# Optimization experiments

Measured on AMD Instinct MI355X. Metric: run time of the kernel, lower is better.

Reference implementation:

```python
import jax, jax.numpy as jnp
import numpy as np

TOP_K = 2


def setup_inputs() -> dict:
    key = jax.random.key(0)
    k0, k1, k2, k3, k4 = jax.random.split(key, 5)
    B, S, H, I, E = 4, 2048, 1024, 2816, 8
    s_h = 1.0 / np.sqrt(H)
    s_i = 1.0 / np.sqrt(I)
    return {
        "x": jax.random.normal(k0, (B, S, H), jnp.float32),
        # nn.Linear weights are stored as [out_features, in_features]
        "w_router": jax.random.normal(k1, (E, H), jnp.float32) * s_h,   # gate: H -> E
        "w_gate": jax.random.normal(k2, (E, I, H), jnp.float32) * s_h,  # per-expert gate_proj
        "w_up": jax.random.normal(k3, (E, I, H), jnp.float32) * s_h,    # per-expert up_proj
        "w_down": jax.random.normal(k4, (E, H, I), jnp.float32) * s_i,  # per-expert down_proj
    }


def reference(x, w_router, w_gate, w_up, w_down):
    B, S, H = x.shape
    E = w_router.shape[0]
    xf = x.reshape(-1, H)                      # [T, H], T = B*S

    # --- Router: softmax over experts, top-k, renormalize weights ---
    logits = jnp.einsum("th,eh->te", xf, w_router)        # [T, E]
    probs = jax.nn.softmax(logits, axis=-1)
    topw, topi = jax.lax.top_k(probs, TOP_K)              # [T, k]
    topw = topw / jnp.sum(topw, axis=-1, keepdims=True)

    # Per-token combine weight for each expert: sum_k w[t,k] * 1[idx[t,k]==e]
    onehot = (topi[..., None] == jnp.arange(E)).astype(x.dtype)  # [T, k, E]
    combine = jnp.einsum("tk,tke->te", topw, onehot)             # [T, E]

    # --- Experts: SwiGLU MLP per expert on all tokens, masked combine ---
    # (masked-dense in the original == gather-compute mathematically,
    # since silu(0)*0 = 0 and the projections have no bias)
    gate = jax.nn.silu(jnp.einsum("th,eih->eti", xf, w_gate))    # [E, T, I]
    up = jnp.einsum("th,eih->eti", xf, w_up)                     # [E, T, I]
    down = jnp.einsum("eti,ehi->eth", gate * up, w_down)         # [E, T, H]

    out = jnp.einsum("eth,te->th", down, combine)                # [T, H]
    return out.reshape(B, S, H)
```

## Files before the change

### kernel.cpp

```cpp
#include <hip/hip_runtime.h>

#define TT 8192
#define HD 1024
#define ID 2816
#define NE 8
#define NID2 (2*ID)

typedef __attribute__((ext_vector_type(8))) short short8;
typedef __attribute__((ext_vector_type(4))) float f32x4;

#define WS_TOP2I 0
#define WS_TOP2W 65536
#define WS_CNT   131072
#define WS_OFF   131136
#define WS_CUR   131200
#define WS_TMAP  131328
#define WS_SLOTW 196864
#define WS_T2S   262400
#define WS_XB    1048576ULL
#define WS_WGU   (WS_XB  + 16777216ULL)
#define WS_WDB   (WS_WGU + 92274688ULL)
#define WS_ACT   (WS_WDB + 46137344ULL)

__device__ __forceinline__ unsigned int pack_bf2(float lo, float hi) {
  unsigned int ul = __builtin_bit_cast(unsigned int, lo) + 0x8000u;
  unsigned int uh = __builtin_bit_cast(unsigned int, hi) + 0x8000u;
  return (uh & 0xffff0000u) | (ul >> 16);
}

__device__ __forceinline__ unsigned short f2bf(float f) {
  unsigned int u = __builtin_bit_cast(unsigned int, f);
  return (unsigned short)((u + 0x8000u) >> 16);
}

__device__ __forceinline__ float bf2f(unsigned short b) {
  unsigned int u = ((unsigned int)b) << 16;
  return __builtin_bit_cast(float, u);
}

__device__ __forceinline__ void gload16(const void* g, void* l) {
  __builtin_amdgcn_global_load_lds(
      (const __attribute__((address_space(1))) unsigned int*)g,
      (__attribute__((address_space(3))) unsigned int*)l, 16, 0, 0);
}

__global__ __launch_bounds__(256) void router_kernel(
    const float* __restrict__ x, const float* __restrict__ wr,
    int* __restrict__ top2i, float* __restrict__ top2w,
    unsigned short* __restrict__ xb)
{
  int tid  = threadIdx.x;
  int lane = tid & 63;
  int t    = blockIdx.x * 4 + (tid >> 6);

  const float4* xp = (const float4*)(x + (size_t)t * HD + lane * 16);
  float4 xv[4];
  #pragma unroll
  for (int j = 0; j < 4; ++j) xv[j] = xp[j];

  uint4 v0, v1;
  v0.x = pack_bf2(xv[0].x, xv[0].y); v0.y = pack_bf2(xv[0].z, xv[0].w);
  v0.z = pack_bf2(xv[1].x, xv[1].y); v0.w = pack_bf2(xv[1].z, xv[1].w);
  v1.x = pack_bf2(xv[2].x, xv[2].y); v1.y = pack_bf2(xv[2].z, xv[2].w);
  v1.z = pack_bf2(xv[3].x, xv[3].y); v1.w = pack_bf2(xv[3].z, xv[3].w);
  uint4* xrow = (uint4*)(xb + (size_t)t * HD + lane * 16);
  xrow[0] = v0; xrow[1] = v1;

  float acc[NE];
  #pragma unroll
  for (int e = 0; e < NE; ++e) {
    const float4* wp = (const float4*)(wr + (size_t)e * HD + lane * 16);
    float s = 0.f;
    #pragma unroll
    for (int j = 0; j < 4; ++j) {
      float4 w = wp[j];
      s += xv[j].x * w.x + xv[j].y * w.y + xv[j].z * w.z + xv[j].w * w.w;
    }
    acc[e] = s;
  }
  #pragma unroll
  for (int d = 1; d < 64; d <<= 1) {
    #pragma unroll
    for (int e = 0; e < NE; ++e) acc[e] += __shfl_xor(acc[e], d, 64);
  }
  int   i0 = 0; float m0 = acc[0];
  #pragma unroll
  for (int e = 1; e < NE; ++e) if (acc[e] > m0) { m0 = acc[e]; i0 = e; }
  int   i1 = -1; float m1 = -3.4e38f;
  #pragma unroll
  for (int e = 0; e < NE; ++e) if (e != i0 && acc[e] > m1) { m1 = acc[e]; i1 = e; }

  float e1 = __expf(m1 - m0);
  float w0 = 1.f / (1.f + e1);
  float w1 = e1 * w0;

  if (lane == 0) {
    top2i[2 * t] = i0;  top2i[2 * t + 1] = i1;
    top2w[2 * t] = w0;  top2w[2 * t + 1] = w1;
  }
}

__global__ __launch_bounds__(256) void count_scan_kernel(
    const int* __restrict__ top2i,
    int* __restrict__ counts, int* __restrict__ offsets, int* __restrict__ cursors)
{
  __shared__ int s_cnt[NE];
  int tid = threadIdx.x;
  if (tid < NE) s_cnt[tid] = 0;
  __syncthreads();

  int c0=0,c1=0,c2=0,c3=0,c4=0,c5=0,c6=0,c7=0;
  for (int t = tid; t < TT; t += 256) {
    int e0 = top2i[2 * t], e1 = top2i[2 * t + 1];
    c0 += __popcll(__ballot(e0 == 0)) + __popcll(__ballot(e1 == 0));
    c1 += __popcll(__ballot(e0 == 1)) + __popcll(__ballot(e1 == 1));
    c2 += __popcll(__ballot(e0 == 2)) + __popcll(__ballot(e1 == 2));
    c3 += __popcll(__ballot(e0 == 3)) + __popcll(__ballot(e1 == 3));
    c4 += __popcll(__ballot(e0 == 4)) + __popcll(__ballot(e1 == 4));
    c5 += __popcll(__ballot(e0 == 5)) + __popcll(__ballot(e1 == 5));
    c6 += __popcll(__ballot(e0 == 6)) + __popcll(__ballot(e1 == 6));
    c7 += __popcll(__ballot(e0 == 7)) + __popcll(__ballot(e1 == 7));
  }
  if ((tid & 63) == 0) {
    atomicAdd(&s_cnt[0], c0); atomicAdd(&s_cnt[1], c1);
    atomicAdd(&s_cnt[2], c2); atomicAdd(&s_cnt[3], c3);
    atomicAdd(&s_cnt[4], c4); atomicAdd(&s_cnt[5], c5);
    atomicAdd(&s_cnt[6], c6); atomicAdd(&s_cnt[7], c7);
  }
  __syncthreads();
  if (tid == 0) {
    int run = 0;
    #pragma unroll
    for (int e = 0; e < NE; ++e) {
      counts[e] = s_cnt[e]; offsets[e] = run; cursors[e] = run; run += s_cnt[e];
    }
    offsets[NE] = run;
  }
}

__global__ __launch_bounds__(256) void place_kernel(
    const int* __restrict__ top2i, const float* __restrict__ top2w,
    int* __restrict__ cursors,
    int* __restrict__ token_map, float* __restrict__ slot_w, int* __restrict__ tok2slot)
{
  int tid  = threadIdx.x;
  int lane = tid & 63;
  int t    = blockIdx.x * 256 + tid;

  #pragma unroll
  for (int k = 0; k < 2; ++k) {
    int   e = top2i[2 * t + k];
    float w = top2w[2 * t + k];
    #pragma unroll
    for (int ee = 0; ee < NE; ++ee) {
      unsigned long long m = __ballot(e == ee);
      if (e == ee) {
        int leader = __ffsll((long long)m) - 1;
        int pre    = __popcll(m & ((1ull << lane) - 1ull));
        int base   = 0;
        if (lane == leader) base = atomicAdd(&cursors[ee], (int)__popcll(m));
        base = __shfl(base, leader, 64);
        token_map[base + pre] = t;
        slot_w[base + pre]    = w;
        tok2slot[2 * t + k]   = base + pre;
      }
    }
  }
}

__global__ __launch_bounds__(256) void cvt_wgu_kernel(
    const float* __restrict__ wg, const float* __restrict__ wu,
    unsigned short* __restrict__ wgu)
{
  int e    = blockIdx.y;
  int idx  = blockIdx.x * 256 + threadIdx.x;
  int col8 = idx & 127;
  int rr   = idx >> 7;
  int blk  = rr >> 5;
  int win  = rr & 31;
  const float* srow = (win < 16)
      ? wg + ((size_t)e * ID + blk * 16 + win) * HD
      : wu + ((size_t)e * ID + blk * 16 + (win - 16)) * HD;
  const float4* p = (const float4*)(srow + col8 * 8);
  float4 a = p[0], b = p[1];
  uint4 v;
  v.x = pack_bf2(a.x, a.y); v.y = pack_bf2(a.z, a.w);
  v.z = pack_bf2(b.x, b.y); v.w = pack_bf2(b.z, b.w);
  *(uint4*)(wgu + ((size_t)e * NID2 + rr) * HD + col8 * 8) = v;
}

__global__ __launch_bounds__(256) void cvt_bf16_kernel(
    const float* __restrict__ in, unsigned short* __restrict__ out, int n8)
{
  int i = blockIdx.x * 256 + threadIdx.x;
  if (i >= n8) return;
  const float4* p = (const float4*)(in + (size_t)i * 8);
  float4 a = p[0], b = p[1];
  uint4 v;
  v.x = pack_bf2(a.x, a.y); v.y = pack_bf2(a.z, a.w);
  v.z = pack_bf2(b.x, b.y); v.w = pack_bf2(b.z, b.w);
  ((uint4*)out)[i] = v;
}


#define STG(kt) { \
    size_t k1 = (size_t)((kt) * 64); \
    char* db = ldsc + (unsigned)tid * 16; \
    _Pragma("unroll") for (int c = 0; c < 4; ++c) { \
      gload16(aS[c] + k1, db + c * 4096); \
      gload16(bS[c] + k1, db + 16384 + c * 4096); } }

#define CMP() { \
    const char* sa = ldsc; \
    const char* sb = ldsc + 16384; \
    _Pragma("unroll") for (int kk = 0; kk < 2; ++kk) { \
      int kb = kk * 64 + kq; \
      short8 af[4], bfr[4]; \
      _Pragma("unroll") for (int n = 0; n < 4; ++n) \
        bfr[n] = *(const short8*)(sb + (wcn * 64 + n * 16 + arow) * 128 + (kb ^ rxor)); \
      _Pragma("unroll") for (int m = 0; m < 4; ++m) \
        af[m] = *(const short8*)(sa + (wr * 64 + m * 16 + arow) * 128 + (kb ^ rxor)); \
      __builtin_amdgcn_s_setprio(1); \
      _Pragma("unroll") for (int m = 0; m < 4; ++m) \
        _Pragma("unroll") for (int n = 0; n < 4; ++n) \
          acc[m][n] = __builtin_amdgcn_mfma_f32_16x16x32_bf16(af[m], bfr[n], acc[m][n], 0, 0, 0); \
      __builtin_amdgcn_s_setprio(0); \
    } }

#define KLOOP(NT) { \
    for (int kt = 0; kt < (NT); ++kt) { \
      if (kt) __syncthreads(); \
      STG(kt); \
      __syncthreads(); \
      CMP(); \
    } }

#define XCD_DECODE(NX, NY) \
  int nwg  = (NX) * (NY) * NE; \
  int flat = blockIdx.x + (NX) * (blockIdx.y + (NY) * blockIdx.z); \
  int qq   = nwg >> 3; \
  int wg   = (flat & 7) * qq + (flat >> 3); \
  int bx   = wg % (NX); \
  int rem  = wg / (NX); \
  int y    = rem % (NY); \
  int e    = rem / (NY);

__global__ __launch_bounds__(256, 2) void gemm1_fast(
    const unsigned short* __restrict__ xb, const unsigned short* __restrict__ wgu,
    const int* __restrict__ counts, const int* __restrict__ offsets,
    const int* __restrict__ token_map, unsigned short* __restrict__ act)
{
  __shared__ __align__(16) char smem[32768];
  char* ldsc = smem;

  XCD_DECODE(16, 44)
  int cnt = counts[e];
  int off = offsets[e];

  int tid  = threadIdx.x;
  int lane = tid & 63;
  int w    = tid >> 6;
  int wr   = w >> 1;
  int wcn  = w & 1;

  int sr8  = tid >> 3;
  int colE = (((tid & 7) ^ (sr8 & 7)) << 3);
  int rxor = (lane & 7) << 4;
  int arow = lane & 15;
  int kq   = (lane >> 4) << 4;
  int prow = (lane >> 4) << 2;

  for (int t0 = bx * 128; t0 < cnt; t0 += 2048) {
    const unsigned short* aS[4];
    const unsigned short* bS[4];
    #pragma unroll
    for (int c = 0; c < 4; ++c) {
      int rowA = t0 + c * 32 + sr8;
      int slot = off + (rowA < cnt ? rowA : cnt - 1);
      aS[c] = xb  + (size_t)token_map[slot] * HD + colE;
      bS[c] = wgu + ((size_t)e * NID2 + (size_t)y * 128 + c * 32 + sr8) * HD + colE;
    }

    f32x4 zf = {0.f, 0.f, 0.f, 0.f};
    f32x4 acc[4][4];
    #pragma unroll
    for (int m = 0; m < 4; ++m)
      #pragma unroll
      for (int n = 0; n < 4; ++n) acc[m][n] = zf;

    KLOOP(HD / 64);

    #pragma unroll
    for (int m = 0; m < 4; ++m) {
      #pragma unroll
      for (int r = 0; r < 4; ++r) {
        int row = wr * 64 + m * 16 + prow + r;
        int tr2 = t0 + row;
        if (tr2 >= cnt) continue;
        size_t ob = (size_t)(off + tr2) * ID + (size_t)y * 64 + wcn * 32 + arow;
        #pragma unroll
        for (int p = 0; p < 2; ++p) {
          float g = acc[m][2 * p][r];
          float u = acc[m][2 * p + 1][r];
          float h = g * u / (1.f + __expf(-g));
          act[ob + p * 16] = f2bf(h);
        }
      }
    }
    __syncthreads();
  }
}


#define STG2(t) { \
    size_t k1 = (size_t)((t) * 64); \
    char* db = ldsc + (((t) & 1) ? 65536u : 0u) + (unsigned)tid * 16; \
    gload16(aS[0] + k1, db);           gload16(aS[1] + k1, db + 8192); \
    gload16(aS[2] + k1, db + 16384);   gload16(aS[3] + k1, db + 24576); \
    gload16(bS[0] + k1, db + 32768);   gload16(bS[1] + k1, db + 40960); \
    gload16(bS[2] + k1, db + 49152);   gload16(bS[3] + k1, db + 57344); }

#define KBODY2(t, NKT) { \
    if ((t) + 1 < (NKT)) STG2((t) + 1); \
    const char* sa = ldsc + (((t) & 1) ? 65536u : 0u); \
    const char* sb = sa + 32768; \
    _Pragma("unroll") for (int kk = 0; kk < 2; ++kk) { \
      int kb = kk * 64 + kq; \
      short8 bfr[4], af[8]; \
      _Pragma("unroll") for (int n = 0; n < 4; ++n) \
        bfr[n] = *(const short8*)(sb + (wc * 64 + n * 16 + arow) * 128 + (kb ^ rxor)); \
      _Pragma("unroll") for (int m = 0; m < 8; ++m) \
        af[m] = *(const short8*)(sa + (wr * 128 + m * 16 + arow) * 128 + (kb ^ rxor)); \
      __builtin_amdgcn_s_setprio(1); \
      _Pragma("unroll") for (int m = 0; m < 8; ++m) \
        _Pragma("unroll") for (int n = 0; n < 4; ++n) \
          acc[m][n] = __builtin_amdgcn_mfma_f32_16x16x32_bf16(af[m], bfr[n], acc[m][n], 0, 0, 0); \
      __builtin_amdgcn_s_setprio(0); \
    } \
    asm volatile("s_waitcnt vmcnt(0)" ::: "memory"); \
    __builtin_amdgcn_s_barrier(); }

__global__ __launch_bounds__(512, 2) void gemm2_fast(
    const unsigned short* __restrict__ act, const unsigned short* __restrict__ wdb,
    const int* __restrict__ counts, const int* __restrict__ offsets,
    unsigned short* __restrict__ down)
{
  extern __shared__ char smem2[];
  char* ldsc = smem2;

  XCD_DECODE(16, 4)
  int cnt = counts[e];
  int off = offsets[e];

  int tid  = threadIdx.x;
  int lane = tid & 63;
  int w    = tid >> 6;
  int wr   = w >> 2;
  int wc   = w & 3;

  int srow0 = tid >> 3;
  int colE  = (((tid & 7) ^ ((tid >> 3) & 7)) << 3);
  int rxor  = (lane & 7) << 4;
  int arow  = lane & 15;
  int kq    = (lane >> 4) << 4;
  int prow  = (lane >> 4) << 2;

  for (int t0 = bx * 256; t0 < cnt; t0 += 4096) {
    const unsigned short* aS[4];
    const unsigned short* bS[4];
    #pragma unroll
    for (int j = 0; j < 4; ++j) {
      int row  = srow0 + 64 * j;
      int tr   = t0 + row;
      int slot = off + (tr < cnt ? tr : cnt - 1);
      aS[j] = act + (size_t)slot * ID + colE;
      bS[j] = wdb + ((size_t)e * HD + (size_t)y * 256 + row) * ID + colE;
    }

    f32x4 zf = {0.f, 0.f, 0.f, 0.f};
    f32x4 acc[8][4];
    #pragma unroll
    for (int m = 0; m < 8; ++m)
      #pragma unroll
      for (int n = 0; n < 4; ++n) acc[m][n] = zf;

    STG2(0);
    asm volatile("s_waitcnt vmcnt(0)" ::: "memory");
    __builtin_amdgcn_s_barrier();
    for (int t = 0; t < ID / 64; ++t) KBODY2(t, ID / 64);

    #pragma unroll
    for (int m = 0; m < 8; ++m) {
      #pragma unroll
      for (int r = 0; r < 4; ++r) {
        int row = wr * 128 + m * 16 + prow + r;
        int tr2 = t0 + row;
        if (tr2 >= cnt) continue;
        unsigned short* ob = down + (size_t)(off + tr2) * HD + (size_t)y * 256 + wc * 64 + arow;
        #pragma unroll
        for (int n = 0; n < 4; ++n)
          ob[n * 16] = f2bf(acc[m][n][r]);
      }
    }
    __syncthreads();
  }
}

__global__ __launch_bounds__(256) void combine_kernel(
    const unsigned short* __restrict__ down, const float* __restrict__ slot_w,
    const int* __restrict__ tok2slot, float* __restrict__ out)
{
  int t   = blockIdx.x;
  int tid = threadIdx.x;
  int s0  = tok2slot[2 * t], s1 = tok2slot[2 * t + 1];
  float w0 = slot_w[s0], w1 = slot_w[s1];
  short8 a = ((const short8*)(down + (size_t)s0 * HD))[tid >> 1 == tid / 2 ? tid : tid];
  if (tid >= HD / 8) return;
  a = ((const short8*)(down + (size_t)s0 * HD))[tid];
  short8 b = ((const short8*)(down + (size_t)s1 * HD))[tid];
  float4 o0, o1;
  float* op = out + (size_t)t * HD + tid * 8;
  #pragma unroll
  for (int j = 0; j < 8; ++j) {
    float va = bf2f((unsigned short)a[j]);
    float vb = bf2f((unsigned short)b[j]);
    op[j] = w0 * va + w1 * vb;
  }
  (void)o0; (void)o1;
}

extern "C" void kernel_launch(void* const* d_in, const int* in_sizes, int n_in,
                              void* d_out, int out_size, void* d_ws, size_t ws_size,
                              hipStream_t stream) {
  const float* x        = (const float*)d_in[0];
  const float* w_router = (const float*)d_in[1];
  const float* w_gate   = (const float*)d_in[2];
  const float* w_up     = (const float*)d_in[3];
  const float* w_down   = (const float*)d_in[4];

  char* ws = (char*)d_ws;
  int*   top2i    = (int*)(ws + WS_TOP2I);
  float* top2w    = (float*)(ws + WS_TOP2W);
  int*   counts   = (int*)(ws + WS_CNT);
  int*   offsets  = (int*)(ws + WS_OFF);
  int*   cursors  = (int*)(ws + WS_CUR);
  int*   tmap     = (int*)(ws + WS_TMAP);
  float* slotw    = (float*)(ws + WS_SLOTW);
  int*   tok2slot = (int*)(ws + WS_T2S);
  unsigned short* xb  = (unsigned short*)(ws + WS_XB);
  unsigned short* wgu = (unsigned short*)(ws + WS_WGU);
  unsigned short* wdb = (unsigned short*)(ws + WS_WDB);
  unsigned short* act = (unsigned short*)(ws + WS_ACT);
  unsigned short* down = (unsigned short*)(ws + WS_WGU);

  hipFuncSetAttribute((const void*)gemm2_fast,
                      hipFuncAttributeMaxDynamicSharedMemorySize, 131072);

  router_kernel<<<TT / 4, 256, 0, stream>>>(x, w_router, top2i, top2w, xb);
  count_scan_kernel<<<1, 256, 0, stream>>>(top2i, counts, offsets, cursors);
  place_kernel<<<TT / 256, 256, 0, stream>>>(top2i, top2w, cursors, tmap, slotw, tok2slot);
  cvt_wgu_kernel<<<dim3(2816, NE), 256, 0, stream>>>(w_gate, w_up, wgu);
  cvt_bf16_kernel<<<11264, 256, 0, stream>>>(w_down, wdb, NE * HD * ID / 8);

  gemm1_fast<<<dim3(16, 44, NE), 256, 0, stream>>>(xb, wgu, counts, offsets, tmap, act);
  gemm2_fast<<<dim3(16, 4, NE), 512, 131072, stream>>>(act, wdb, counts, offsets, down);
  combine_kernel<<<TT, 256, 0, stream>>>(down, slotw, tok2slot, (float*)d_out);
}
```

Before: 529.2 us.

## Double-buffer LDS in gemm1 K-loop and shrink combine blocks

The gemm1 K-loop now uses two 32KB LDS buffers. Each iteration issues the global-to-LDS loads for the next K tile before running MFMAs on the current one, then waits on vmcnt and hits a single barrier, where before it had two syncs per tile with no overlap. LDS per block doubles to 64KB, which may limit occupancy under launch_bounds(256,2). Separately, combine_kernel launches 128 threads per token, matching the work, instead of 256 threads of which half idled after a redundant load.

Result: slower. 541.3 us (+2.3%).

```diff
diff --git a/kernel.cpp b/kernel.cpp
--- a/kernel.cpp
+++ b/kernel.cpp
@@ -203,16 +203,17 @@
 }
 
 
-#define STG(kt) { \
+#define STG1(kt) { \
     size_t k1 = (size_t)((kt) * 64); \
-    char* db = ldsc + (unsigned)tid * 16; \
+    char* db = ldsc + (((kt) & 1) ? 32768u : 0u) + (unsigned)tid * 16; \
     _Pragma("unroll") for (int c = 0; c < 4; ++c) { \
       gload16(aS[c] + k1, db + c * 4096); \
       gload16(bS[c] + k1, db + 16384 + c * 4096); } }
 
-#define CMP() { \
-    const char* sa = ldsc; \
-    const char* sb = ldsc + 16384; \
+#define KBODY1(t, NT) { \
+    if ((t) + 1 < (NT)) STG1((t) + 1); \
+    const char* sa = ldsc + (((t) & 1) ? 32768u : 0u); \
+    const char* sb = sa + 16384; \
     _Pragma("unroll") for (int kk = 0; kk < 2; ++kk) { \
       int kb = kk * 64 + kq; \
       short8 af[4], bfr[4]; \
@@ -225,15 +226,9 @@
         _Pragma("unroll") for (int n = 0; n < 4; ++n) \
           acc[m][n] = __builtin_amdgcn_mfma_f32_16x16x32_bf16(af[m], bfr[n], acc[m][n], 0, 0, 0); \
       __builtin_amdgcn_s_setprio(0); \
-    } }
-
-#define KLOOP(NT) { \
-    for (int kt = 0; kt < (NT); ++kt) { \
-      if (kt) __syncthreads(); \
-      STG(kt); \
-      __syncthreads(); \
-      CMP(); \
-    } }
+    } \
+    asm volatile("s_waitcnt vmcnt(0)" ::: "memory"); \
+    __builtin_amdgcn_s_barrier(); }
 
 #define XCD_DECODE(NX, NY) \
   int nwg  = (NX) * (NY) * NE; \
@@ -250,7 +245,7 @@
     const int* __restrict__ counts, const int* __restrict__ offsets,
     const int* __restrict__ token_map, unsigned short* __restrict__ act)
 {
-  __shared__ __align__(16) char smem[32768];
+  __shared__ __align__(16) char smem[65536];
   char* ldsc = smem;
 
   XCD_DECODE(16, 44)
@@ -288,7 +283,10 @@
       #pragma unroll
       for (int n = 0; n < 4; ++n) acc[m][n] = zf;
 
-    KLOOP(HD / 64);
+    STG1(0);
+    asm volatile("s_waitcnt vmcnt(0)" ::: "memory");
+    __builtin_amdgcn_s_barrier();
+    for (int t = 0; t < HD / 64; ++t) KBODY1(t, HD / 64);
 
     #pragma unroll
     for (int m = 0; m < 4; ++m) {
@@ -406,7 +404,7 @@
   }
 }
 
-__global__ __launch_bounds__(256) void combine_kernel(
+__global__ __launch_bounds__(128) void combine_kernel(
     const unsigned short* __restrict__ down, const float* __restrict__ slot_w,
     const int* __restrict__ tok2slot, float* __restrict__ out)
 {
@@ -414,11 +412,8 @@
   int tid = threadIdx.x;
   int s0  = tok2slot[2 * t], s1 = tok2slot[2 * t + 1];
   float w0 = slot_w[s0], w1 = slot_w[s1];
-  short8 a = ((const short8*)(down + (size_t)s0 * HD))[tid >> 1 == tid / 2 ? tid : tid];
-  if (tid >= HD / 8) return;
-  a = ((const short8*)(down + (size_t)s0 * HD))[tid];
+  short8 a = ((const short8*)(down + (size_t)s0 * HD))[tid];
   short8 b = ((const short8*)(down + (size_t)s1 * HD))[tid];
-  float4 o0, o1;
   float* op = out + (size_t)t * HD + tid * 8;
   #pragma unroll
   for (int j = 0; j < 8; ++j) {
@@ -426,7 +421,6 @@
     float vb = bf2f((unsigned short)b[j]);
     op[j] = w0 * va + w1 * vb;
   }
-  (void)o0; (void)o1;
 }
 
 extern "C" void kernel_launch(void* const* d_in, const int* in_sizes, int n_in,
@@ -464,5 +458,5 @@
 
   gemm1_fast<<<dim3(16, 44, NE), 256, 0, stream>>>(xb, wgu, counts, offsets, tmap, act);
   gemm2_fast<<<dim3(16, 4, NE), 512, 131072, stream>>>(act, wdb, counts, offsets, down);
-  combine_kernel<<<TT, 256, 0, stream>>>(down, slotw, tok2slot, (float*)d_out);
-}
+  combine_kernel<<<TT, 128, 0, stream>>>(down, slotw, tok2slot, (float*)d_out);
+}
```
